# Optimization experiments

Measured on AMD Instinct MI355X. Metric: run time of the kernel, lower is better.

The kernel has to match this reference:

```python
import jax, jax.numpy as jnp
import numpy as np

B, T = 8, 512
N_QUBITS, N_ROT, D_PER = 64, 16, 64
D = N_QUBITS * D_PER


def setup_inputs() -> dict:
    key = jax.random.key(0)
    k1, k2, k3, k4 = jax.random.split(key, 4)
    return {
        "x": jax.random.normal(k1, (B, T, D), dtype=jnp.float32),
        "rx_params": jax.random.normal(k2, (N_QUBITS, N_ROT), dtype=jnp.float32),
        "ry_params": jax.random.normal(k3, (N_QUBITS, N_ROT), dtype=jnp.float32),
        "rz_params": jax.random.normal(k4, (N_QUBITS, N_ROT), dtype=jnp.float32),
    }


def _rot_diag(theta, axis):
    # theta: (Q,) per-qubit angle. The torch einsum 'btqd,btqq->btqd' only uses
    # the diagonal of the (Q,Q) rotation matrix. For rx/ry, the paired-qubit
    # construction puts cos(theta_k/2) on both diagonal slots of pair k
    # (first Q//2 angles are used, matching cos[..., :len(idx)]).
    Q = theta.shape[0]
    half = theta[: Q // 2] * 0.5
    if axis in ("x", "y"):
        return jnp.repeat(jnp.cos(half).astype(jnp.complex64), 2)
    # rz: diag(exp(-i a/2), exp(+i a/2)) interleaved over pairs
    e = jnp.exp(-1j * half.astype(jnp.complex64))
    return jnp.stack([e, jnp.conj(e)], axis=-1).reshape(-1)


def _apply_rotation(state, theta, axis):
    # state: (B, T, Q, d_per) complex64
    sf = jnp.fft.fft2(state, axes=(-2, -1))
    sf = sf * _rot_diag(theta, axis)[:, None]  # diagonal per-qubit scale
    return jnp.fft.ifft2(sf, axes=(-2, -1)).real  # torch takes .real


def reference(x, rx_params, ry_params, rz_params):
    b, t, d = x.shape
    q = rx_params.shape[0]
    state = x.reshape(b, t, q, d // q).astype(jnp.complex64)
    for params, axis in ((rx_params, "x"), (ry_params, "y"), (rz_params, "z")):
        theta = params.sum(-1)  # combine n_rotations into one angle per qubit
        state = _apply_rotation(state, theta, axis).astype(jnp.complex64)
    state = state.reshape(b, t, d)
    # noise model: (1 + amp_noise) * exp(i * phase_noise) * state, then L2 norm
    ka, kp = jax.random.split(jax.random.key(42))
    amp = 0.01 * jax.random.normal(ka, state.shape, dtype=jnp.float32)
    ph = 0.005 * jax.random.normal(kp, state.shape, dtype=jnp.float32)
    noisy = (1.0 + amp) * jnp.exp(1j * ph.astype(jnp.complex64)) * state
    norm = jnp.linalg.norm(noisy, axis=-1, keepdims=True)
    noisy = noisy / (norm + 1e-8)
    return jnp.abs(noisy)  # measurement
```

## Files before the change

### kernel.cpp

```cpp
#include <hip/hip_runtime.h>
#include <stdint.h>

typedef _Float16 half8 __attribute__((ext_vector_type(8)));
typedef float floatx4 __attribute__((ext_vector_type(4)));

__device__ __forceinline__ uint32_t rotl32(uint32_t v, int r) {
  return (v << r) | (v >> (32 - r));
}

__device__ __forceinline__ void threefry2x32(uint32_t k0, uint32_t k1,
                                             uint32_t x0, uint32_t x1,
                                             uint32_t& o0, uint32_t& o1) {
  uint32_t k2 = k0 ^ k1 ^ 0x1BD11BDAu;
  x0 += k0; x1 += k1;
#define TF_R(r) { x0 += x1; x1 = rotl32(x1, (r)); x1 ^= x0; }
  TF_R(13) TF_R(15) TF_R(26) TF_R(6)   x0 += k1; x1 += k2 + 1u;
  TF_R(17) TF_R(29) TF_R(16) TF_R(24)  x0 += k2; x1 += k0 + 2u;
  TF_R(13) TF_R(15) TF_R(26) TF_R(6)   x0 += k0; x1 += k1 + 3u;
  TF_R(17) TF_R(29) TF_R(16) TF_R(24)  x0 += k1; x1 += k2 + 4u;
  TF_R(13) TF_R(15) TF_R(26) TF_R(6)   x0 += k2; x1 += k0 + 5u;
#undef TF_R
  o0 = x0; o1 = x1;
}

__device__ __forceinline__ float erfinv_fast(float x) {
  float w = -__logf(fmaf(-x, x, 1.0f));
  float p;
  if (w < 5.0f) {
    w = w - 2.5f;
    p = 2.81022636e-08f;
    p = fmaf(p, w, 3.43273939e-07f);
    p = fmaf(p, w, -3.5233877e-06f);
    p = fmaf(p, w, -4.39150654e-06f);
    p = fmaf(p, w, 0.00021858087f);
    p = fmaf(p, w, -0.00125372503f);
    p = fmaf(p, w, -0.00417768164f);
    p = fmaf(p, w, 0.246640727f);
    p = fmaf(p, w, 1.50140941f);
  } else {
    w = sqrtf(w) - 3.0f;
    p = -0.000200214257f;
    p = fmaf(p, w, 0.000100950558f);
    p = fmaf(p, w, 0.00134934322f);
    p = fmaf(p, w, -0.00367342844f);
    p = fmaf(p, w, 0.00573950773f);
    p = fmaf(p, w, -0.0076224613f);
    p = fmaf(p, w, 0.00943887047f);
    p = fmaf(p, w, 1.00167406f);
    p = fmaf(p, w, 2.83297682f);
  }
  return p * x;
}

__device__ __align__(16) _Float16 grevh2[128];
__device__ uint32_t g_key[2];

__global__ void setup_kernel(const float* __restrict__ rx,
                             const float* __restrict__ ry,
                             const float* __restrict__ rz) {
  __shared__ float cre[3][64], cim[3][64];
  __shared__ float Gr[64], Gi[64];
  __shared__ float twc[64], tws[64];
  __shared__ float gs[64];
  const int t = threadIdx.x;

  if (t < 32) {
    const float* ps[3] = {rx, ry, rz};
    for (int a = 0; a < 3; ++a) {
      float s = 0.0f;
      for (int r = 0; r < 16; ++r) s += ps[a][t * 16 + r];
      float h = 0.5f * s;
      float ch = cosf(h), sh = sinf(h);
      if (a < 2) {
        cre[a][2 * t] = ch;     cim[a][2 * t] = 0.0f;
        cre[a][2 * t + 1] = ch; cim[a][2 * t + 1] = 0.0f;
      } else {
        cre[2][2 * t] = ch;     cim[2][2 * t] = -sh;
        cre[2][2 * t + 1] = ch; cim[2][2 * t + 1] = sh;
      }
    }
  }
  {
    double ang = (2.0 * 3.14159265358979323846 / 64.0) * (double)t;
    twc[t] = (float)cos(ang);
    tws[t] = (float)sin(ang);
  }
  __syncthreads();

  {
    const int k = t, kn = (64 - k) & 63;
    float pr = 1.0f, pi = 0.0f;
    for (int a = 0; a < 3; ++a) {
      float cr = 0.5f * (cre[a][k] + cre[a][kn]);
      float ci = 0.5f * (cim[a][k] - cim[a][kn]);
      float nr = pr * cr - pi * ci;
      float ni = pr * ci + pi * cr;
      pr = nr; pi = ni;
    }
    Gr[k] = pr; Gi[k] = pi;
  }
  __syncthreads();

  {
    const int mi = t;
    float s = 0.0f;
    for (int k = 0; k < 64; ++k) {
      int idx = (k * mi) & 63;
      s = fmaf(Gr[k], twc[idx], s);
      s = fmaf(-Gi[k], tws[idx], s);
    }
    gs[mi] = s * (1.0f / 64.0f);
  }
  __syncthreads();

  {
    _Float16 hv = (_Float16)gs[(64 - t) & 63];
    grevh2[t] = hv;
    grevh2[t + 64] = hv;
  }

  if (t == 0) {
    uint32_t o0, o1;
    threefry2x32(0u, 42u, 0u, 0u, o0, o1);
    g_key[0] = o0; g_key[1] = o1;
  }
}

__global__ __launch_bounds__(256, 5) void qmain(const float* __restrict__ x,
                                                float* __restrict__ out) {
  __shared__ __align__(16) _Float16 Xt[64 * 72];
  __shared__ float red[4];
  const int tid = threadIdx.x;
  const int row = blockIdx.x;
  const int lane = tid & 63;
  const int w = tid >> 6;
  const int quad = lane >> 4;
  const int m = lane & 15;

  half8 af0, af1;
  {
    const int s0 = (8 * quad - 16 * w - m) & 63;
    const int s1 = (32 + 8 * quad - 16 * w - m) & 63;
#pragma unroll
    for (int j = 0; j < 8; ++j) af0[j] = grevh2[s0 + j];
#pragma unroll
    for (int j = 0; j < 8; ++j) af1[j] = grevh2[s1 + j];
  }
  const uint32_t ka0 = g_key[0], ka1 = g_key[1];

  {
    const float* xr = x + (size_t)row * 4096;
    const int tq = tid >> 4;
    const int d0 = (tid & 15) * 4;
#pragma unroll
    for (int u = 0; u < 2; ++u) {
      const int q0 = 2 * tq + 32 * u;
      float4 a = *(const float4*)(xr + q0 * 64 + d0);
      float4 b = *(const float4*)(xr + (q0 + 1) * 64 + d0);
      const float av[4] = {a.x, a.y, a.z, a.w};
      const float bv[4] = {b.x, b.y, b.z, b.w};
#pragma unroll
      for (int i = 0; i < 4; ++i) {
        union { _Float16 h[2]; uint32_t u32; } pk;
        pk.h[0] = (_Float16)av[i];
        pk.h[1] = (_Float16)bv[i];
        *(uint32_t*)&Xt[(d0 + i) * 72 + q0] = pk.u32;
      }
    }
  }
  __syncthreads();

  floatx4 acc[4];
#pragma unroll
  for (int c = 0; c < 4; ++c) {
    const _Float16* bp = &Xt[(16 * c + m) * 72 + 8 * quad];
    half8 b0 = *(const half8*)bp;
    half8 b1 = *(const half8*)(bp + 32);
    acc[c] = (floatx4){0.0f, 0.0f, 0.0f, 0.0f};
    acc[c] = __builtin_amdgcn_mfma_f32_16x16x32_f16(af0, b0, acc[c], 0, 0, 0);
    acc[c] = __builtin_amdgcn_mfma_f32_16x16x32_f16(af1, b1, acc[c], 0, 0, 0);
  }

  const uint32_t idxbase = ((uint32_t)row << 12) + (uint32_t)(((16 * w + 4 * quad) << 6) + m);
  float wabs[16];
  float ssum = 0.0f;
#pragma unroll
  for (int c = 0; c < 4; ++c) {
#pragma unroll
    for (int r = 0; r < 4; ++r) {
      const uint32_t idx = idxbase + (uint32_t)(r * 64 + 16 * c);
      uint32_t o0, o1;
      threefry2x32(ka0, ka1, 0u, idx, o0, o1);
      uint32_t bits = o0 ^ o1;
      float f = __uint_as_float((bits >> 9) | 0x3f800000u) - 1.0f;
      const float lo = -0.99999994f;
      float u = fmaxf(fmaf(f, 2.0f, lo), lo);
      float z = 1.41421356237309515f * erfinv_fast(u);
      float wv = fmaf(0.01f, z, 1.0f) * acc[c][r];
      ssum = fmaf(wv, wv, ssum);
      wabs[c * 4 + r] = fabsf(wv);
    }
  }

#pragma unroll
  for (int off = 32; off >= 1; off >>= 1) ssum += __shfl_xor(ssum, off, 64);
  if (lane == 0) red[w] = ssum;
  __syncthreads();
  const float total = red[0] + red[1] + red[2] + red[3];
  const float scale = 1.0f / (sqrtf(total) + 1e-8f);

  float* ob = out + (size_t)row * 4096 + (size_t)(((16 * w + 4 * quad) << 6) + m);
#pragma unroll
  for (int c = 0; c < 4; ++c)
#pragma unroll
    for (int r = 0; r < 4; ++r)
      ob[r * 64 + 16 * c] = wabs[c * 4 + r] * scale;
}

extern "C" void kernel_launch(void* const* d_in, const int* in_sizes, int n_in,
                              void* d_out, int out_size, void* d_ws, size_t ws_size,
                              hipStream_t stream) {
  const float* x  = (const float*)d_in[0];
  const float* rx = (const float*)d_in[1];
  const float* ry = (const float*)d_in[2];
  const float* rz = (const float*)d_in[3];
  float* out = (float*)d_out;

  setup_kernel<<<1, 64, 0, stream>>>(rx, ry, rz);
  qmain<<<4096, 256, 0, stream>>>(x, out);
}
```

Measured before the change: 142.6 us.

## Precompute per-thread MFMA A-fragments, widen transposed LDS stores, raise occupancy

The setup kernel now runs with 256 threads and writes a ready-made 16-half A fragment for every thread of qmain, so each thread loads its MFMA operands with two vector reads instead of sixteen scalar gathers. The x-to-LDS transpose now packs eight rows into 128-bit stores rather than 32-bit ones. Launch bounds go from 5 to 8 waves, and the noise math is folded into fewer ops with the rare erfinv branch marked unlikely. The higher occupancy target may force register spills.

```diff
diff --git a/kernel.cpp b/kernel.cpp
--- a/kernel.cpp
+++ b/kernel.cpp
@@ -26,7 +26,18 @@
 __device__ __forceinline__ float erfinv_fast(float x) {
   float w = -__logf(fmaf(-x, x, 1.0f));
   float p;
-  if (w < 5.0f) {
+  if (__builtin_expect(w >= 5.0f, 0)) {
+    w = sqrtf(w) - 3.0f;
+    p = -0.000200214257f;
+    p = fmaf(p, w, 0.000100950558f);
+    p = fmaf(p, w, 0.00134934322f);
+    p = fmaf(p, w, -0.00367342844f);
+    p = fmaf(p, w, 0.00573950773f);
+    p = fmaf(p, w, -0.0076224613f);
+    p = fmaf(p, w, 0.00943887047f);
+    p = fmaf(p, w, 1.00167406f);
+    p = fmaf(p, w, 2.83297682f);
+  } else {
     w = w - 2.5f;
     p = 2.81022636e-08f;
     p = fmaf(p, w, 3.43273939e-07f);
@@ -37,22 +48,11 @@
     p = fmaf(p, w, -0.00417768164f);
     p = fmaf(p, w, 0.246640727f);
     p = fmaf(p, w, 1.50140941f);
-  } else {
-    w = sqrtf(w) - 3.0f;
-    p = -0.000200214257f;
-    p = fmaf(p, w, 0.000100950558f);
-    p = fmaf(p, w, 0.00134934322f);
-    p = fmaf(p, w, -0.00367342844f);
-    p = fmaf(p, w, 0.00573950773f);
-    p = fmaf(p, w, -0.0076224613f);
-    p = fmaf(p, w, 0.00943887047f);
-    p = fmaf(p, w, 1.00167406f);
-    p = fmaf(p, w, 2.83297682f);
   }
   return p * x;
 }
 
-__device__ __align__(16) _Float16 grevh2[128];
+__device__ __align__(16) _Float16 g_afrag[256 * 16];
 __device__ uint32_t g_key[2];
 
 __global__ void setup_kernel(const float* __restrict__ rx,
@@ -80,14 +80,14 @@
       }
     }
   }
-  {
+  if (t < 64) {
     double ang = (2.0 * 3.14159265358979323846 / 64.0) * (double)t;
     twc[t] = (float)cos(ang);
     tws[t] = (float)sin(ang);
   }
   __syncthreads();
 
-  {
+  if (t < 64) {
     const int k = t, kn = (64 - k) & 63;
     float pr = 1.0f, pi = 0.0f;
     for (int a = 0; a < 3; ++a) {
@@ -101,7 +101,7 @@
   }
   __syncthreads();
 
-  {
+  if (t < 64) {
     const int mi = t;
     float s = 0.0f;
     for (int k = 0; k < 64; ++k) {
@@ -114,9 +114,13 @@
   __syncthreads();
 
   {
-    _Float16 hv = (_Float16)gs[(64 - t) & 63];
-    grevh2[t] = hv;
-    grevh2[t + 64] = hv;
+    const int w = t >> 6, lane = t & 63, quad = lane >> 4, m = lane & 15;
+    const int r0 = 16 * w + m - 8 * quad;
+#pragma unroll
+    for (int j = 0; j < 8; ++j) {
+      g_afrag[t * 16 + j]     = (_Float16)gs[(r0 - j) & 63];
+      g_afrag[t * 16 + 8 + j] = (_Float16)gs[(r0 - 32 - j) & 63];
+    }
   }
 
   if (t == 0) {
@@ -126,7 +130,7 @@
   }
 }
 
-__global__ __launch_bounds__(256, 5) void qmain(const float* __restrict__ x,
+__global__ __launch_bounds__(256, 8) void qmain(const float* __restrict__ x,
                                                 float* __restrict__ out) {
   __shared__ __align__(16) _Float16 Xt[64 * 72];
   __shared__ float red[4];
@@ -137,36 +141,23 @@
   const int quad = lane >> 4;
   const int m = lane & 15;
 
-  half8 af0, af1;
-  {
-    const int s0 = (8 * quad - 16 * w - m) & 63;
-    const int s1 = (32 + 8 * quad - 16 * w - m) & 63;
-#pragma unroll
-    for (int j = 0; j < 8; ++j) af0[j] = grevh2[s0 + j];
-#pragma unroll
-    for (int j = 0; j < 8; ++j) af1[j] = grevh2[s1 + j];
-  }
+  const half8* at = (const half8*)g_afrag;
+  half8 af0 = at[2 * tid];
+  half8 af1 = at[2 * tid + 1];
   const uint32_t ka0 = g_key[0], ka1 = g_key[1];
 
   {
     const float* xr = x + (size_t)row * 4096;
-    const int tq = tid >> 4;
-    const int d0 = (tid & 15) * 4;
-#pragma unroll
-    for (int u = 0; u < 2; ++u) {
-      const int q0 = 2 * tq + 32 * u;
-      float4 a = *(const float4*)(xr + q0 * 64 + d0);
-      float4 b = *(const float4*)(xr + (q0 + 1) * 64 + d0);
-      const float av[4] = {a.x, a.y, a.z, a.w};
-      const float bv[4] = {b.x, b.y, b.z, b.w};
-#pragma unroll
-      for (int i = 0; i < 4; ++i) {
-        union { _Float16 h[2]; uint32_t u32; } pk;
-        pk.h[0] = (_Float16)av[i];
-        pk.h[1] = (_Float16)bv[i];
-        *(uint32_t*)&Xt[(d0 + i) * 72 + q0] = pk.u32;
-      }
-    }
+    const int d0 = (tid & 31) * 2;
+    const int q0 = (tid >> 5) * 8;
+    float2 v[8];
+#pragma unroll
+    for (int s = 0; s < 8; ++s) v[s] = *(const float2*)(xr + (q0 + s) * 64 + d0);
+    union { _Float16 h[8]; uint4 u; } r0, r1;
+#pragma unroll
+    for (int s = 0; s < 8; ++s) { r0.h[s] = (_Float16)v[s].x; r1.h[s] = (_Float16)v[s].y; }
+    *(uint4*)&Xt[d0 * 72 + q0] = r0.u;
+    *(uint4*)&Xt[(d0 + 1) * 72 + q0] = r1.u;
   }
   __syncthreads();
 
@@ -182,7 +173,7 @@
   }
 
   const uint32_t idxbase = ((uint32_t)row << 12) + (uint32_t)(((16 * w + 4 * quad) << 6) + m);
-  float wabs[16];
+  float wv[16];
   float ssum = 0.0f;
 #pragma unroll
   for (int c = 0; c < 4; ++c) {
@@ -192,13 +183,11 @@
       uint32_t o0, o1;
       threefry2x32(ka0, ka1, 0u, idx, o0, o1);
       uint32_t bits = o0 ^ o1;
-      float f = __uint_as_float((bits >> 9) | 0x3f800000u) - 1.0f;
-      const float lo = -0.99999994f;
-      float u = fmaxf(fmaf(f, 2.0f, lo), lo);
-      float z = 1.41421356237309515f * erfinv_fast(u);
-      float wv = fmaf(0.01f, z, 1.0f) * acc[c][r];
-      ssum = fmaf(wv, wv, ssum);
-      wabs[c * 4 + r] = fabsf(wv);
+      float vf = __uint_as_float((bits >> 9) | 0x3f800000u);
+      float u = fmaxf(fmaf(vf, 2.0f, -3.0f), -0.99999994f);
+      float val = fmaf(erfinv_fast(u), 0.014142135623730951f, 1.0f) * acc[c][r];
+      ssum = fmaf(val, val, ssum);
+      wv[c * 4 + r] = val;
     }
   }
 
@@ -214,7 +203,7 @@
   for (int c = 0; c < 4; ++c)
 #pragma unroll
     for (int r = 0; r < 4; ++r)
-      ob[r * 64 + 16 * c] = wabs[c * 4 + r] * scale;
+      ob[r * 64 + 16 * c] = fabsf(wv[c * 4 + r]) * scale;
 }
 
 extern "C" void kernel_launch(void* const* d_in, const int* in_sizes, int n_in,
@@ -226,6 +215,6 @@
   const float* rz = (const float*)d_in[3];
   float* out = (float*)d_out;
 
-  setup_kernel<<<1, 64, 0, stream>>>(rx, ry, rz);
+  setup_kernel<<<1, 256, 0, stream>>>(rx, ry, rz);
   qmain<<<4096, 256, 0, stream>>>(x, out);
 }
```

New measurement: 141.0 us. No clear change (-1.1%).
